# Kernel tuning notes

Measured on AMD Instinct MI355X. Metric: run time of the kernel, lower is better.

The kernel has to match this reference:

```python
import jax, jax.numpy as jnp
import numpy as np

TAU = 0.07  # temperature from init_kwargs


def setup_inputs() -> dict:
    key = jax.random.key(0)
    k1, k2 = jax.random.split(key)
    B, D, NUM_CLASSES = 8192, 128, 10
    emb = jax.random.normal(k1, (B, D), dtype=jnp.float32)
    # module assumes L2-normalised embeddings (inner product == cosine sim)
    emb = emb / jnp.linalg.norm(emb, axis=1, keepdims=True)
    labels = jax.random.randint(k2, (B,), 0, NUM_CLASSES, dtype=jnp.int64)
    return {"embeddings": emb, "labels": labels}


def reference(embeddings, labels):
    B = embeddings.shape[0]
    sim = (embeddings @ embeddings.T) / TAU  # [B, B]
    eye = jnp.eye(B, dtype=bool)
    pos_mask = (labels[:, None] == labels[None, :]) & ~eye  # [B, B]
    # denominator excludes self-similarity
    log_denom = jax.nn.logsumexp(jnp.where(eye, -jnp.inf, sim), axis=1)  # [B]
    n_pos = jnp.sum(pos_mask, axis=1)  # [B] int
    pos_sum = jnp.sum(jnp.where(pos_mask, sim, 0.0), axis=1)  # [B]
    has_pos = n_pos > 0
    # loss_i = -mean_p (sim[i,p] - log_denom[i]) = -(pos_sum/n - log_denom)
    loss_i = -(pos_sum / jnp.maximum(n_pos, 1).astype(sim.dtype) - log_denom)
    n_anchors = jnp.maximum(jnp.sum(has_pos), 1).astype(sim.dtype)
    return jnp.sum(jnp.where(has_pos, loss_i, 0.0)) / n_anchors
```

## Files before the change

kernel.cpp:

```cpp
#include <hip/hip_runtime.h>
#include <stdint.h>

typedef unsigned short ushort_t;
typedef __bf16 bf16x8 __attribute__((ext_vector_type(8)));
typedef float f32x4 __attribute__((ext_vector_type(4)));
typedef unsigned short u16x8 __attribute__((ext_vector_type(8)));

#define TAU_F 0.07f
#define C2F 20.60992915555662f
#define INV_TAU 14.285714285714286f

#if __has_builtin(__builtin_amdgcn_exp2f)
#define EXP2F(x) __builtin_amdgcn_exp2f(x)
#else
#define EXP2F(x) exp2f(x)
#endif

#define A_OFF     0u
#define LSUM_OFF  2097152u
#define S_OFF     2359296u
#define CNT_OFF   2364416u
#define CBLK_OFF  2364480u

__device__ __forceinline__ ushort_t f2bf(float x) {
  uint32_t u = __float_as_uint(x);
  u += 0x7FFFu + ((u >> 16) & 1u);
  return (ushort_t)(u >> 16);
}

__device__ __forceinline__ void gll16(const void* g, void* l) {
  __builtin_amdgcn_global_load_lds(
      (const __attribute__((address_space(1))) uint32_t*)g,
      (__attribute__((address_space(3))) uint32_t*)l, 16, 0, 0);
}

__global__ __launch_bounds__(256) void k_prep(const float* __restrict__ emb,
                                              const int* __restrict__ labels,
                                              ushort_t* __restrict__ abf,
                                              float* __restrict__ S,
                                              int* __restrict__ cnt) {
  __shared__ float ssh[1280];
  __shared__ int csh[16];
  const int tid = threadIdx.x, b = blockIdx.x;
  for (int i = tid; i < 1280; i += 256) ssh[i] = 0.f;
  if (tid < 16) csh[tid] = 0;
  __syncthreads();

  const int r = b * 32 + (tid >> 3);
  const int c0 = (tid & 7) * 16;
  const int lab = labels[r];
  const float4* src = (const float4*)(emb + (size_t)r * 128 + c0);
  float v[16];
#pragma unroll
  for (int q = 0; q < 4; ++q) {
    float4 f = src[q];
    v[q * 4 + 0] = f.x; v[q * 4 + 1] = f.y; v[q * 4 + 2] = f.z; v[q * 4 + 3] = f.w;
  }
  u16x8 o0, o1;
#pragma unroll
  for (int k = 0; k < 8; ++k) { o0[k] = f2bf(v[k]); o1[k] = f2bf(v[8 + k]); }
  *(u16x8*)(abf + (size_t)r * 128 + c0) = o0;
  *(u16x8*)(abf + (size_t)r * 128 + c0 + 8) = o1;

#pragma unroll
  for (int k = 0; k < 16; ++k) atomicAdd(&ssh[lab * 128 + c0 + k], v[k]);
  if (c0 == 0) atomicAdd(&csh[lab], 1);
  __syncthreads();

  for (int i = tid; i < 1280; i += 256) atomicAdd(&S[i], ssh[i]);
  if (tid < 16 && csh[tid] != 0) atomicAdd(&cnt[tid], csh[tid]);
}

__global__ __launch_bounds__(512, 2) void k_main(const ushort_t* __restrict__ abf,
                                                 float* __restrict__ lsum_out) {
  __shared__ __attribute__((aligned(16))) char lds[131072];
  const int tid = threadIdx.x;
  const int lane = tid & 63;
  const int wave = tid >> 6;
  const int lo = lane & 15, hi = lane >> 4;
  const int wr = wave >> 1, wc = wave & 1;
  const int band = blockIdx.x & 31;
  const int slice = blockIdx.x >> 5;
  const int row0 = band * 256;
  const int col0 = slice * 1024;

#pragma unroll
  for (int i = 0; i < 8; ++i) {
    int p = i * 512 + tid;
    int r = p >> 4, s = p & 15;
    const ushort_t* g = abf + (size_t)(row0 + r) * 128 + ((s ^ (r & 7)) << 3);
    gll16(g, lds + (size_t)(i * 512 + wave * 64) * 16);
  }
#pragma unroll
  for (int i = 0; i < 4; ++i) {
    int p = i * 512 + tid;
    int r = p >> 4, s = p & 15;
    const ushort_t* g = abf + (size_t)(col0 + r) * 128 + ((s ^ (r & 7)) << 3);
    gll16(g, lds + 65536 + (size_t)(i * 512 + wave * 64) * 16);
  }
  asm volatile("s_waitcnt vmcnt(0)" ::: "memory");
  __builtin_amdgcn_s_barrier();
  __builtin_amdgcn_sched_barrier(0);

  bf16x8 af[4][4];
#pragma unroll
  for (int mf = 0; mf < 4; ++mf) {
#pragma unroll
    for (int ks = 0; ks < 4; ++ks) {
      int r = wr * 64 + mf * 16 + lo;
      int kb = ks * 64 + hi * 16;
      af[mf][ks] = *(const bf16x8*)(lds + r * 256 + (kb ^ ((r & 7) << 4)));
    }
  }

  float lsum[4][4];
#pragma unroll
  for (int mf = 0; mf < 4; ++mf)
#pragma unroll
    for (int q = 0; q < 4; ++q) lsum[mf][q] = 0.f;

  int cur = 0;
  for (int t = 0; t < 8; ++t) {
    if (t < 7) {
      const int tc0 = col0 + (t + 1) * 128;
      char* buf = lds + 65536 + (cur ^ 1) * 32768;
#pragma unroll
      for (int i = 0; i < 4; ++i) {
        int p = i * 512 + tid;
        int r = p >> 4, s = p & 15;
        const ushort_t* g = abf + (size_t)(tc0 + r) * 128 + ((s ^ (r & 7)) << 3);
        gll16(g, buf + (size_t)(i * 512 + wave * 64) * 16);
      }
    }
    const char* bb = lds + 65536 + cur * 32768;
    f32x4 acc[4][4];
    const f32x4 z = {0.f, 0.f, 0.f, 0.f};
#pragma unroll
    for (int mf = 0; mf < 4; ++mf)
#pragma unroll
      for (int nf = 0; nf < 4; ++nf) acc[mf][nf] = z;

#pragma unroll
    for (int ks = 0; ks < 4; ++ks) {
      bf16x8 bfr[4];
#pragma unroll
      for (int nf = 0; nf < 4; ++nf) {
        int c = wc * 64 + nf * 16 + lo;
        int kb = ks * 64 + hi * 16;
        bfr[nf] = *(const bf16x8*)(bb + c * 256 + (kb ^ ((c & 7) << 4)));
      }
#pragma unroll
      for (int mf = 0; mf < 4; ++mf)
#pragma unroll
        for (int nf = 0; nf < 4; ++nf)
          acc[mf][nf] = __builtin_amdgcn_mfma_f32_16x16x32_bf16(
              af[mf][ks], bfr[nf], acc[mf][nf], 0, 0, 0);
    }

    const int gr0 = row0 + wr * 64;
    const int gc0 = col0 + t * 128 + wc * 64;
    const bool diag = (gr0 == gc0);
#pragma unroll
    for (int mf = 0; mf < 4; ++mf) {
#pragma unroll
      for (int nf = 0; nf < 4; ++nf) {
#pragma unroll
        for (int q = 0; q < 4; ++q) {
          float d = acc[mf][nf][q];
          float e = EXP2F(fmaf(d, C2F, -C2F));
          if (diag && (mf * 16 + hi * 4 + q) == (nf * 16 + lo)) e = 0.f;
          lsum[mf][q] += e;
        }
      }
    }

    asm volatile("s_waitcnt vmcnt(0)" ::: "memory");
    __builtin_amdgcn_s_barrier();
    __builtin_amdgcn_sched_barrier(0);
    cur ^= 1;
  }

#pragma unroll
  for (int mf = 0; mf < 4; ++mf) {
#pragma unroll
    for (int q = 0; q < 4; ++q) {
      float v = lsum[mf][q];
      v += __shfl_xor(v, 1);
      v += __shfl_xor(v, 2);
      v += __shfl_xor(v, 4);
      v += __shfl_xor(v, 8);
      lsum[mf][q] = v;
    }
  }
  float* lsh = (float*)lds;
  __syncthreads();
  if (lo == 0 && wc == 0) {
#pragma unroll
    for (int mf = 0; mf < 4; ++mf)
#pragma unroll
      for (int q = 0; q < 4; ++q)
        lsh[wr * 64 + mf * 16 + hi * 4 + q] = lsum[mf][q];
  }
  __syncthreads();
  if (lo == 0 && wc == 1) {
#pragma unroll
    for (int mf = 0; mf < 4; ++mf)
#pragma unroll
      for (int q = 0; q < 4; ++q)
        lsh[wr * 64 + mf * 16 + hi * 4 + q] += lsum[mf][q];
  }
  __syncthreads();
  if (tid < 256) lsum_out[(size_t)slice * 8192 + row0 + tid] = lsh[tid];
}

__global__ __launch_bounds__(256) void k_row(const float* __restrict__ emb,
                                             const int* __restrict__ labels,
                                             const float* __restrict__ S,
                                             const int* __restrict__ cnt,
                                             const float* __restrict__ lsum_part,
                                             float* __restrict__ cblk) {
  const int tid = threadIdx.x;
  const int lane = tid & 63;
  const int w = tid >> 6;
  const int i = blockIdx.x * 4 + w;
  const int lab = labels[i];
  float2 a = ((const float2*)(emb + (size_t)i * 128))[lane];
  float2 s = ((const float2*)(S + (size_t)lab * 128))[lane];
  float pd = a.x * s.x + a.y * s.y;
  float sd = a.x * a.x + a.y * a.y;
#pragma unroll
  for (int m = 1; m < 64; m <<= 1) { pd += __shfl_xor(pd, m); sd += __shfl_xor(sd, m); }
  float ls = (lane < 8) ? lsum_part[(size_t)lane * 8192 + i] : 0.f;
  ls += __shfl_xor(ls, 1); ls += __shfl_xor(ls, 2); ls += __shfl_xor(ls, 4);

  float loss = 0.f, anc = 0.f;
  if (lane == 0) {
    int np = cnt[lab] - 1;
    float logden = logf(ls) + INV_TAU;
    if (np > 0) {
      loss = logden - (pd - sd) / (TAU_F * (float)np);
      anc = 1.f;
    }
  }
  __shared__ float red[8];
  if (lane == 0) { red[w * 2] = loss; red[w * 2 + 1] = anc; }
  __syncthreads();
  if (tid == 0) {
    cblk[(size_t)blockIdx.x * 2]     = red[0] + red[2] + red[4] + red[6];
    cblk[(size_t)blockIdx.x * 2 + 1] = red[1] + red[3] + red[5] + red[7];
  }
}

__global__ __launch_bounds__(256) void k_fin(const float* __restrict__ cblk,
                                             float* __restrict__ out) {
  const int tid = threadIdx.x;
  float sl = 0.f, sa = 0.f;
  for (int i = tid; i < 2048; i += 256) { sl += cblk[i * 2]; sa += cblk[i * 2 + 1]; }
  __shared__ float shl[256], sha[256];
  shl[tid] = sl; sha[tid] = sa;
  __syncthreads();
  for (int s = 128; s > 0; s >>= 1) {
    if (tid < s) { shl[tid] += shl[tid + s]; sha[tid] += sha[tid + s]; }
    __syncthreads();
  }
  if (tid == 0) out[0] = shl[0] / fmaxf(sha[0], 1.0f);
}

extern "C" void kernel_launch(void* const* d_in, const int* in_sizes, int n_in,
                              void* d_out, int out_size, void* d_ws, size_t ws_size,
                              hipStream_t stream) {
  const float* emb = (const float*)d_in[0];
  const int* labels = (const int*)d_in[1];
  char* ws = (char*)d_ws;
  ushort_t* abf = (ushort_t*)(ws + A_OFF);
  float* lsum  = (float*)(ws + LSUM_OFF);
  float* S     = (float*)(ws + S_OFF);
  int*   cnt   = (int*)(ws + CNT_OFF);
  float* cblk  = (float*)(ws + CBLK_OFF);
  float* out   = (float*)d_out;

  hipMemsetAsync(ws + S_OFF, 0, 5184, stream);
  hipLaunchKernelGGL(k_prep, dim3(256), dim3(256), 0, stream, emb, labels, abf, S, cnt);
  hipLaunchKernelGGL(k_main, dim3(256), dim3(512), 0, stream, abf, lsum);
  hipLaunchKernelGGL(k_row, dim3(2048), dim3(256), 0, stream, emb, labels, S, cnt, lsum, cblk);
  hipLaunchKernelGGL(k_fin, dim3(1), dim3(256), 0, stream, cblk, out);
}
```

Measured before the change: 99.13 us.

## Fuse prep, main, row and final kernels into one persistent kernel with grid barriers

Merges the four separate kernel launches into a single 256-block persistent kernel. Software grid barriers built on global atomic counters order the bf16 conversion and class-sum phase, the similarity/logsumexp phase and the per-row loss phase. The final reduction becomes a global atomic accumulate, with the last-arriving block writing the output. This removes launch overhead and inter-kernel gaps, but depends on all 256 blocks being co-resident and adds spin-wait barrier costs.

```diff
diff --git a/kernel.cpp b/kernel.cpp
--- a/kernel.cpp
+++ b/kernel.cpp
@@ -9,6 +9,7 @@
 #define TAU_F 0.07f
 #define C2F 20.60992915555662f
 #define INV_TAU 14.285714285714286f
+#define NBLK 256u
 
 #if __has_builtin(__builtin_amdgcn_exp2f)
 #define EXP2F(x) __builtin_amdgcn_exp2f(x)
@@ -20,7 +21,9 @@
 #define LSUM_OFF  2097152u
 #define S_OFF     2359296u
 #define CNT_OFF   2364416u
-#define CBLK_OFF  2364480u
+#define BAR_OFF   2364480u
+#define ACC_OFF   2364544u
+#define ZERO_LEN  5312u
 
 __device__ __forceinline__ ushort_t f2bf(float x) {
   uint32_t u = __float_as_uint(x);
@@ -34,236 +37,247 @@
       (__attribute__((address_space(3))) uint32_t*)l, 16, 0, 0);
 }
 
-__global__ __launch_bounds__(256) void k_prep(const float* __restrict__ emb,
-                                              const int* __restrict__ labels,
-                                              ushort_t* __restrict__ abf,
-                                              float* __restrict__ S,
-                                              int* __restrict__ cnt) {
-  __shared__ float ssh[1280];
-  __shared__ int csh[16];
-  const int tid = threadIdx.x, b = blockIdx.x;
-  for (int i = tid; i < 1280; i += 256) ssh[i] = 0.f;
-  if (tid < 16) csh[tid] = 0;
+__device__ __forceinline__ void gridbar(uint32_t* ctr) {
+  __threadfence();
   __syncthreads();
-
-  const int r = b * 32 + (tid >> 3);
-  const int c0 = (tid & 7) * 16;
-  const int lab = labels[r];
-  const float4* src = (const float4*)(emb + (size_t)r * 128 + c0);
-  float v[16];
-#pragma unroll
-  for (int q = 0; q < 4; ++q) {
-    float4 f = src[q];
-    v[q * 4 + 0] = f.x; v[q * 4 + 1] = f.y; v[q * 4 + 2] = f.z; v[q * 4 + 3] = f.w;
+  if (threadIdx.x == 0) {
+    atomicAdd(ctr, 1u);
+    while (__hip_atomic_load(ctr, __ATOMIC_RELAXED, __HIP_MEMORY_SCOPE_AGENT) < NBLK)
+      __builtin_amdgcn_s_sleep(1);
   }
-  u16x8 o0, o1;
-#pragma unroll
-  for (int k = 0; k < 8; ++k) { o0[k] = f2bf(v[k]); o1[k] = f2bf(v[8 + k]); }
-  *(u16x8*)(abf + (size_t)r * 128 + c0) = o0;
-  *(u16x8*)(abf + (size_t)r * 128 + c0 + 8) = o1;
-
-#pragma unroll
-  for (int k = 0; k < 16; ++k) atomicAdd(&ssh[lab * 128 + c0 + k], v[k]);
-  if (c0 == 0) atomicAdd(&csh[lab], 1);
   __syncthreads();
-
-  for (int i = tid; i < 1280; i += 256) atomicAdd(&S[i], ssh[i]);
-  if (tid < 16 && csh[tid] != 0) atomicAdd(&cnt[tid], csh[tid]);
-}
-
-__global__ __launch_bounds__(512, 2) void k_main(const ushort_t* __restrict__ abf,
-                                                 float* __restrict__ lsum_out) {
+  __threadfence();
+}
+
+__global__ __launch_bounds__(512, 2) void k_fused(const float* __restrict__ emb,
+                                                  const int* __restrict__ labels,
+                                                  ushort_t* __restrict__ abf,
+                                                  float* __restrict__ lsum_out,
+                                                  float* __restrict__ S,
+                                                  int* __restrict__ cnt,
+                                                  uint32_t* __restrict__ bar,
+                                                  float* __restrict__ acc,
+                                                  float* __restrict__ out) {
   __shared__ __attribute__((aligned(16))) char lds[131072];
   const int tid = threadIdx.x;
-  const int lane = tid & 63;
-  const int wave = tid >> 6;
-  const int lo = lane & 15, hi = lane >> 4;
-  const int wr = wave >> 1, wc = wave & 1;
-  const int band = blockIdx.x & 31;
-  const int slice = blockIdx.x >> 5;
-  const int row0 = band * 256;
-  const int col0 = slice * 1024;
-
-#pragma unroll
-  for (int i = 0; i < 8; ++i) {
-    int p = i * 512 + tid;
-    int r = p >> 4, s = p & 15;
-    const ushort_t* g = abf + (size_t)(row0 + r) * 128 + ((s ^ (r & 7)) << 3);
-    gll16(g, lds + (size_t)(i * 512 + wave * 64) * 16);
+  const int b = blockIdx.x;
+
+  {
+    float* ssh = (float*)lds;
+    int* csh = (int*)(lds + 5120);
+    for (int i = tid; i < 1280; i += 512) ssh[i] = 0.f;
+    if (tid < 16) csh[tid] = 0;
+    __syncthreads();
+
+    const int r = b * 32 + (tid >> 4);
+    const int c0 = (tid & 15) * 8;
+    const int lab = labels[r];
+    float4 f0 = *(const float4*)(emb + (size_t)r * 128 + c0);
+    float4 f1 = *(const float4*)(emb + (size_t)r * 128 + c0 + 4);
+    u16x8 o;
+    o[0] = f2bf(f0.x); o[1] = f2bf(f0.y); o[2] = f2bf(f0.z); o[3] = f2bf(f0.w);
+    o[4] = f2bf(f1.x); o[5] = f2bf(f1.y); o[6] = f2bf(f1.z); o[7] = f2bf(f1.w);
+    *(u16x8*)(abf + (size_t)r * 128 + c0) = o;
+
+    atomicAdd(&ssh[lab * 128 + c0 + 0], f0.x);
+    atomicAdd(&ssh[lab * 128 + c0 + 1], f0.y);
+    atomicAdd(&ssh[lab * 128 + c0 + 2], f0.z);
+    atomicAdd(&ssh[lab * 128 + c0 + 3], f0.w);
+    atomicAdd(&ssh[lab * 128 + c0 + 4], f1.x);
+    atomicAdd(&ssh[lab * 128 + c0 + 5], f1.y);
+    atomicAdd(&ssh[lab * 128 + c0 + 6], f1.z);
+    atomicAdd(&ssh[lab * 128 + c0 + 7], f1.w);
+    if (c0 == 0) atomicAdd(&csh[lab], 1);
+    __syncthreads();
+
+    for (int i = tid; i < 1280; i += 512) atomicAdd(&S[i], ssh[i]);
+    if (tid < 16 && csh[tid] != 0) atomicAdd(&cnt[tid], csh[tid]);
   }
-#pragma unroll
-  for (int i = 0; i < 4; ++i) {
-    int p = i * 512 + tid;
-    int r = p >> 4, s = p & 15;
-    const ushort_t* g = abf + (size_t)(col0 + r) * 128 + ((s ^ (r & 7)) << 3);
-    gll16(g, lds + 65536 + (size_t)(i * 512 + wave * 64) * 16);
-  }
-  asm volatile("s_waitcnt vmcnt(0)" ::: "memory");
-  __builtin_amdgcn_s_barrier();
-  __builtin_amdgcn_sched_barrier(0);
-
-  bf16x8 af[4][4];
-#pragma unroll
-  for (int mf = 0; mf < 4; ++mf) {
-#pragma unroll
-    for (int ks = 0; ks < 4; ++ks) {
-      int r = wr * 64 + mf * 16 + lo;
-      int kb = ks * 64 + hi * 16;
-      af[mf][ks] = *(const bf16x8*)(lds + r * 256 + (kb ^ ((r & 7) << 4)));
-    }
-  }
-
-  float lsum[4][4];
-#pragma unroll
-  for (int mf = 0; mf < 4; ++mf)
-#pragma unroll
-    for (int q = 0; q < 4; ++q) lsum[mf][q] = 0.f;
-
-  int cur = 0;
-  for (int t = 0; t < 8; ++t) {
-    if (t < 7) {
-      const int tc0 = col0 + (t + 1) * 128;
-      char* buf = lds + 65536 + (cur ^ 1) * 32768;
-#pragma unroll
-      for (int i = 0; i < 4; ++i) {
-        int p = i * 512 + tid;
-        int r = p >> 4, s = p & 15;
-        const ushort_t* g = abf + (size_t)(tc0 + r) * 128 + ((s ^ (r & 7)) << 3);
-        gll16(g, buf + (size_t)(i * 512 + wave * 64) * 16);
-      }
-    }
-    const char* bb = lds + 65536 + cur * 32768;
-    f32x4 acc[4][4];
-    const f32x4 z = {0.f, 0.f, 0.f, 0.f};
-#pragma unroll
-    for (int mf = 0; mf < 4; ++mf)
-#pragma unroll
-      for (int nf = 0; nf < 4; ++nf) acc[mf][nf] = z;
-
-#pragma unroll
-    for (int ks = 0; ks < 4; ++ks) {
-      bf16x8 bfr[4];
-#pragma unroll
-      for (int nf = 0; nf < 4; ++nf) {
-        int c = wc * 64 + nf * 16 + lo;
-        int kb = ks * 64 + hi * 16;
-        bfr[nf] = *(const bf16x8*)(bb + c * 256 + (kb ^ ((c & 7) << 4)));
-      }
-#pragma unroll
-      for (int mf = 0; mf < 4; ++mf)
-#pragma unroll
-        for (int nf = 0; nf < 4; ++nf)
-          acc[mf][nf] = __builtin_amdgcn_mfma_f32_16x16x32_bf16(
-              af[mf][ks], bfr[nf], acc[mf][nf], 0, 0, 0);
-    }
-
-    const int gr0 = row0 + wr * 64;
-    const int gc0 = col0 + t * 128 + wc * 64;
-    const bool diag = (gr0 == gc0);
-#pragma unroll
-    for (int mf = 0; mf < 4; ++mf) {
-#pragma unroll
-      for (int nf = 0; nf < 4; ++nf) {
-#pragma unroll
-        for (int q = 0; q < 4; ++q) {
-          float d = acc[mf][nf][q];
-          float e = EXP2F(fmaf(d, C2F, -C2F));
-          if (diag && (mf * 16 + hi * 4 + q) == (nf * 16 + lo)) e = 0.f;
-          lsum[mf][q] += e;
-        }
-      }
-    }
-
+  gridbar(bar + 0);
+
+  {
+    const int lane = tid & 63;
+    const int wave = tid >> 6;
+    const int lo = lane & 15, hi = lane >> 4;
+    const int wr = wave >> 1, wc = wave & 1;
+    const int band = b & 31;
+    const int slice = b >> 5;
+    const int row0 = band * 256;
+    const int col0 = slice * 1024;
+
+#pragma unroll
+    for (int i = 0; i < 8; ++i) {
+      int p = i * 512 + tid;
+      int r = p >> 4, s = p & 15;
+      const ushort_t* g = abf + (size_t)(row0 + r) * 128 + ((s ^ (r & 7)) << 3);
+      gll16(g, lds + (size_t)(i * 512 + wave * 64) * 16);
+    }
+#pragma unroll
+    for (int i = 0; i < 4; ++i) {
+      int p = i * 512 + tid;
+      int r = p >> 4, s = p & 15;
+      const ushort_t* g = abf + (size_t)(col0 + r) * 128 + ((s ^ (r & 7)) << 3);
+      gll16(g, lds + 65536 + (size_t)(i * 512 + wave * 64) * 16);
+    }
     asm volatile("s_waitcnt vmcnt(0)" ::: "memory");
     __builtin_amdgcn_s_barrier();
     __builtin_amdgcn_sched_barrier(0);
-    cur ^= 1;
+
+    bf16x8 af[4][4];
+#pragma unroll
+    for (int mf = 0; mf < 4; ++mf) {
+#pragma unroll
+      for (int ks = 0; ks < 4; ++ks) {
+        int r = wr * 64 + mf * 16 + lo;
+        int kb = ks * 64 + hi * 16;
+        af[mf][ks] = *(const bf16x8*)(lds + r * 256 + (kb ^ ((r & 7) << 4)));
+      }
+    }
+
+    float lsum[4][4];
+#pragma unroll
+    for (int mf = 0; mf < 4; ++mf)
+#pragma unroll
+      for (int q = 0; q < 4; ++q) lsum[mf][q] = 0.f;
+
+    int cur = 0;
+    for (int t = 0; t < 8; ++t) {
+      if (t < 7) {
+        const int tc0 = col0 + (t + 1) * 128;
+        char* buf = lds + 65536 + (cur ^ 1) * 32768;
+#pragma unroll
+        for (int i = 0; i < 4; ++i) {
+          int p = i * 512 + tid;
+          int r = p >> 4, s = p & 15;
+          const ushort_t* g = abf + (size_t)(tc0 + r) * 128 + ((s ^ (r & 7)) << 3);
+          gll16(g, buf + (size_t)(i * 512 + wave * 64) * 16);
+        }
+      }
+      const char* bb = lds + 65536 + cur * 32768;
+      f32x4 acc2[4][4];
+      const f32x4 z = {0.f, 0.f, 0.f, 0.f};
+#pragma unroll
+      for (int mf = 0; mf < 4; ++mf)
+#pragma unroll
+        for (int nf = 0; nf < 4; ++nf) acc2[mf][nf] = z;
+
+#pragma unroll
+      for (int ks = 0; ks < 4; ++ks) {
+        bf16x8 bfr[4];
+#pragma unroll
+        for (int nf = 0; nf < 4; ++nf) {
+          int c = wc * 64 + nf * 16 + lo;
+          int kb = ks * 64 + hi * 16;
+          bfr[nf] = *(const bf16x8*)(bb + c * 256 + (kb ^ ((c & 7) << 4)));
+        }
+#pragma unroll
+        for (int mf = 0; mf < 4; ++mf)
+#pragma unroll
+          for (int nf = 0; nf < 4; ++nf)
+            acc2[mf][nf] = __builtin_amdgcn_mfma_f32_16x16x32_bf16(
+                af[mf][ks], bfr[nf], acc2[mf][nf], 0, 0, 0);
+      }
+
+      const int gr0 = row0 + wr * 64;
+      const int gc0 = col0 + t * 128 + wc * 64;
+      const bool diag = (gr0 == gc0);
+#pragma unroll
+      for (int mf = 0; mf < 4; ++mf) {
+#pragma unroll
+        for (int nf = 0; nf < 4; ++nf) {
+#pragma unroll
+          for (int q = 0; q < 4; ++q) {
+            float d = acc2[mf][nf][q];
+            float e = EXP2F(fmaf(d, C2F, -C2F));
+            if (diag && (mf * 16 + hi * 4 + q) == (nf * 16 + lo)) e = 0.f;
+            lsum[mf][q] += e;
+          }
+        }
+      }
+
+      asm volatile("s_waitcnt vmcnt(0)" ::: "memory");
+      __builtin_amdgcn_s_barrier();
+      __builtin_amdgcn_sched_barrier(0);
+      cur ^= 1;
+    }
+
+#pragma unroll
+    for (int mf = 0; mf < 4; ++mf) {
+#pragma unroll
+      for (int q = 0; q < 4; ++q) {
+        float v = lsum[mf][q];
+        v += __shfl_xor(v, 1);
+        v += __shfl_xor(v, 2);
+        v += __shfl_xor(v, 4);
+        v += __shfl_xor(v, 8);
+        lsum[mf][q] = v;
+      }
+    }
+    float* lsh = (float*)lds;
+    __syncthreads();
+    if (lo == 0 && wc == 0) {
+#pragma unroll
+      for (int mf = 0; mf < 4; ++mf)
+#pragma unroll
+        for (int q = 0; q < 4; ++q)
+          lsh[wr * 64 + mf * 16 + hi * 4 + q] = lsum[mf][q];
+    }
+    __syncthreads();
+    if (lo == 0 && wc == 1) {
+#pragma unroll
+      for (int mf = 0; mf < 4; ++mf)
+#pragma unroll
+        for (int q = 0; q < 4; ++q)
+          lsh[wr * 64 + mf * 16 + hi * 4 + q] += lsum[mf][q];
+    }
+    __syncthreads();
+    if (tid < 256) lsum_out[(size_t)slice * 8192 + row0 + tid] = lsh[tid];
   }
-
-#pragma unroll
-  for (int mf = 0; mf < 4; ++mf) {
-#pragma unroll
-    for (int q = 0; q < 4; ++q) {
-      float v = lsum[mf][q];
-      v += __shfl_xor(v, 1);
-      v += __shfl_xor(v, 2);
-      v += __shfl_xor(v, 4);
-      v += __shfl_xor(v, 8);
-      lsum[mf][q] = v;
+  gridbar(bar + 1);
+
+  {
+    const int lane = tid & 63;
+    const int w = tid >> 6;
+    float lossacc = 0.f, ancacc = 0.f;
+#pragma unroll
+    for (int rr = 0; rr < 4; ++rr) {
+      const int i = b * 32 + w * 4 + rr;
+      const int lab = labels[i];
+      float2 a = ((const float2*)(emb + (size_t)i * 128))[lane];
+      float2 s = ((const float2*)(S + (size_t)lab * 128))[lane];
+      float pd = a.x * s.x + a.y * s.y;
+      float sd = a.x * a.x + a.y * a.y;
+#pragma unroll
+      for (int m = 1; m < 64; m <<= 1) { pd += __shfl_xor(pd, m); sd += __shfl_xor(sd, m); }
+      float ls = (lane < 8) ? lsum_out[(size_t)lane * 8192 + i] : 0.f;
+      ls += __shfl_xor(ls, 1); ls += __shfl_xor(ls, 2); ls += __shfl_xor(ls, 4);
+      if (lane == 0) {
+        int np = cnt[lab] - 1;
+        if (np > 0) {
+          float logden = logf(ls) + INV_TAU;
+          lossacc += logden - (pd - sd) / (TAU_F * (float)np);
+          ancacc += 1.f;
+        }
+      }
+    }
+    float* red = (float*)lds;
+    if (lane == 0) { red[w * 2] = lossacc; red[w * 2 + 1] = ancacc; }
+    __syncthreads();
+    if (tid == 0) {
+      float sl = 0.f, sa = 0.f;
+#pragma unroll
+      for (int k = 0; k < 8; ++k) { sl += red[k * 2]; sa += red[k * 2 + 1]; }
+      atomicAdd(&acc[0], sl);
+      atomicAdd(&acc[1], sa);
+      __threadfence();
+      uint32_t old = atomicAdd(bar + 2, 1u);
+      if (old == NBLK - 1) {
+        float L = __hip_atomic_load(&acc[0], __ATOMIC_RELAXED, __HIP_MEMORY_SCOPE_AGENT);
+        float A = __hip_atomic_load(&acc[1], __ATOMIC_RELAXED, __HIP_MEMORY_SCOPE_AGENT);
+        out[0] = L / fmaxf(A, 1.0f);
+      }
     }
   }
-  float* lsh = (float*)lds;
-  __syncthreads();
-  if (lo == 0 && wc == 0) {
-#pragma unroll
-    for (int mf = 0; mf < 4; ++mf)
-#pragma unroll
-      for (int q = 0; q < 4; ++q)
-        lsh[wr * 64 + mf * 16 + hi * 4 + q] = lsum[mf][q];
-  }
-  __syncthreads();
-  if (lo == 0 && wc == 1) {
-#pragma unroll
-    for (int mf = 0; mf < 4; ++mf)
-#pragma unroll
-      for (int q = 0; q < 4; ++q)
-        lsh[wr * 64 + mf * 16 + hi * 4 + q] += lsum[mf][q];
-  }
-  __syncthreads();
-  if (tid < 256) lsum_out[(size_t)slice * 8192 + row0 + tid] = lsh[tid];
-}
-
-__global__ __launch_bounds__(256) void k_row(const float* __restrict__ emb,
-                                             const int* __restrict__ labels,
-                                             const float* __restrict__ S,
-                                             const int* __restrict__ cnt,
-                                             const float* __restrict__ lsum_part,
-                                             float* __restrict__ cblk) {
-  const int tid = threadIdx.x;
-  const int lane = tid & 63;
-  const int w = tid >> 6;
-  const int i = blockIdx.x * 4 + w;
-  const int lab = labels[i];
-  float2 a = ((const float2*)(emb + (size_t)i * 128))[lane];
-  float2 s = ((const float2*)(S + (size_t)lab * 128))[lane];
-  float pd = a.x * s.x + a.y * s.y;
-  float sd = a.x * a.x + a.y * a.y;
-#pragma unroll
-  for (int m = 1; m < 64; m <<= 1) { pd += __shfl_xor(pd, m); sd += __shfl_xor(sd, m); }
-  float ls = (lane < 8) ? lsum_part[(size_t)lane * 8192 + i] : 0.f;
-  ls += __shfl_xor(ls, 1); ls += __shfl_xor(ls, 2); ls += __shfl_xor(ls, 4);
-
-  float loss = 0.f, anc = 0.f;
-  if (lane == 0) {
-    int np = cnt[lab] - 1;
-    float logden = logf(ls) + INV_TAU;
-    if (np > 0) {
-      loss = logden - (pd - sd) / (TAU_F * (float)np);
-      anc = 1.f;
-    }
-  }
-  __shared__ float red[8];
-  if (lane == 0) { red[w * 2] = loss; red[w * 2 + 1] = anc; }
-  __syncthreads();
-  if (tid == 0) {
-    cblk[(size_t)blockIdx.x * 2]     = red[0] + red[2] + red[4] + red[6];
-    cblk[(size_t)blockIdx.x * 2 + 1] = red[1] + red[3] + red[5] + red[7];
-  }
-}
-
-__global__ __launch_bounds__(256) void k_fin(const float* __restrict__ cblk,
-                                             float* __restrict__ out) {
-  const int tid = threadIdx.x;
-  float sl = 0.f, sa = 0.f;
-  for (int i = tid; i < 2048; i += 256) { sl += cblk[i * 2]; sa += cblk[i * 2 + 1]; }
-  __shared__ float shl[256], sha[256];
-  shl[tid] = sl; sha[tid] = sa;
-  __syncthreads();
-  for (int s = 128; s > 0; s >>= 1) {
-    if (tid < s) { shl[tid] += shl[tid + s]; sha[tid] += sha[tid + s]; }
-    __syncthreads();
-  }
-  if (tid == 0) out[0] = shl[0] / fmaxf(sha[0], 1.0f);
 }
 
 extern "C" void kernel_launch(void* const* d_in, const int* in_sizes, int n_in,
@@ -276,12 +290,11 @@
   float* lsum  = (float*)(ws + LSUM_OFF);
   float* S     = (float*)(ws + S_OFF);
   int*   cnt   = (int*)(ws + CNT_OFF);
-  float* cblk  = (float*)(ws + CBLK_OFF);
+  uint32_t* bar = (uint32_t*)(ws + BAR_OFF);
+  float* acc   = (float*)(ws + ACC_OFF);
   float* out   = (float*)d_out;
 
-  hipMemsetAsync(ws + S_OFF, 0, 5184, stream);
-  hipLaunchKernelGGL(k_prep, dim3(256), dim3(256), 0, stream, emb, labels, abf, S, cnt);
-  hipLaunchKernelGGL(k_main, dim3(256), dim3(512), 0, stream, abf, lsum);
-  hipLaunchKernelGGL(k_row, dim3(2048), dim3(256), 0, stream, emb, labels, S, cnt, lsum, cblk);
-  hipLaunchKernelGGL(k_fin, dim3(1), dim3(256), 0, stream, cblk, out);
-}
+  hipMemsetAsync(ws + S_OFF, 0, ZERO_LEN, stream);
+  hipLaunchKernelGGL(k_fused, dim3(NBLK), dim3(512), 0, stream,
+                     emb, labels, abf, lsum, S, cnt, bar, acc, out);
+}
```

New measurement: 229.4 us. 131% more time.
